# Kernel tuning notes

Measured on AMD Instinct MI355X. Metric: run time of the kernel, lower is better.

## Reference

```python
import jax, jax.numpy as jnp
import numpy as np
from jax import lax

T = 1.0      # terminal time
SIGMA = 1.0  # diffusion coefficient
N, D, P, M, H = 16384, 16, 8, 50, 128


def setup_inputs() -> dict:
    key = jax.random.key(0)
    ks = jax.random.split(key, 8)
    scale1 = 1.0 / np.sqrt(1 + D + P)
    scale2 = 1.0 / np.sqrt(H)
    return {
        "initial_states": jax.random.normal(ks[0], (N, D), jnp.float32),
        "initial_values": jax.random.normal(ks[1], (N,), jnp.float32),
        "observations": jax.random.normal(ks[2], (N, P), jnp.float32),
        "noise": jax.random.normal(ks[3], (M, N, D), jnp.float32),
        "W1": jax.random.normal(ks[4], (1 + D + P, H), jnp.float32) * scale1,
        "b1": jnp.zeros((H,), jnp.float32),
        "W2": jax.random.normal(ks[5], (H, H), jnp.float32) * scale2,
        "b2": jnp.zeros((H,), jnp.float32),
        "W3": jax.random.normal(ks[6], (H, D), jnp.float32) * scale2,
        "b3": jnp.zeros((D,), jnp.float32),
    }


def reference(initial_states, initial_values, observations, noise,
              W1, b1, W2, b2, W3, b3):
    """Euler-Maruyama rollout of simulate_SDEs: joint (X, V) SDE with
    per-step Z-network drift. drift b(X) = -X (OU process)."""
    m_steps = noise.shape[0]
    dt = jnp.asarray(T / m_steps, initial_states.dtype)
    sqrt_dt = jnp.sqrt(dt)
    times = jnp.arange(m_steps, dtype=initial_states.dtype) * dt  # time[m]

    def z_net(t, X, Y):
        tcol = jnp.full((X.shape[0], 1), t, X.dtype)
        h = jnp.concatenate([tcol, X, Y], axis=1)      # (N, 1+d+p)
        h = jax.nn.relu(h @ W1 + b1)
        h = jax.nn.relu(h @ W2 + b2)
        return h @ W3 + b3                             # (N, d)

    def step(carry, inp):
        X, V = carry
        eps, t = inp
        Wn = sqrt_dt * eps                             # Brownian increment
        Z = z_net(t, X, observations)
        drift_V = 0.5 * jnp.sum(Z * Z, axis=1)
        V = V + dt * drift_V + jnp.sum(Z * Wn, axis=1)
        X = X + dt * (-X) + SIGMA * Wn                 # b(X) = -X
        return (X, V), None

    (X, V), _ = lax.scan(step, (initial_states, initial_values), (noise, times))
    return X, V
```

## Files before the change

kernel.cpp:

```cpp
#include <hip/hip_runtime.h>

typedef __bf16   bf16x8 __attribute__((ext_vector_type(8)));
typedef float    f32x4  __attribute__((ext_vector_type(4)));
typedef float    f32x2  __attribute__((ext_vector_type(2)));
typedef uint32_t u32x4  __attribute__((ext_vector_type(4)));

constexpr int N_ = 16384;
constexpr int D_ = 16;
constexpr int P_ = 8;
constexpr int H_ = 128;
constexpr int M_ = 50;

__device__ __forceinline__ uint32_t pk_bf16(float a, float b) {
    uint32_t ua = __builtin_bit_cast(uint32_t, a) + 0x8000u;
    uint32_t ub = __builtin_bit_cast(uint32_t, b) + 0x8000u;
    return __builtin_amdgcn_perm(ub, ua, 0x07060302u);
}
__device__ __forceinline__ uint32_t pk_relu_bf16(float a, float b) {
    return pk_bf16(fmaxf(a, 0.0f), fmaxf(b, 0.0f));
}

__global__ __launch_bounds__(64, 1)
void sde_fused(const float* __restrict__ X0,
               const float* __restrict__ V0,
               const float* __restrict__ Yobs,
               const float* __restrict__ noise,
               const float* __restrict__ W1, const float* __restrict__ b1,
               const float* __restrict__ W2, const float* __restrict__ b2,
               const float* __restrict__ W3, const float* __restrict__ b3,
               float* __restrict__ out)
{
    const int lane = threadIdx.x;
    const int n    = lane & 15;
    const int q    = lane >> 4;
    const int gr   = blockIdx.x * 16 + n;

    const float dt   = 0.02f;
    const float sqdt = 0.1414213562373095f;

    bf16x8 w1f[8];
#pragma unroll
    for (int ct = 0; ct < 8; ++ct) {
        u32x4 u;
        u[0] = pk_bf16(W1[(1 + q * 4 + 0) * H_ + ct * 16 + n],
                       W1[(1 + q * 4 + 1) * H_ + ct * 16 + n]);
        u[1] = pk_bf16(W1[(1 + q * 4 + 2) * H_ + ct * 16 + n],
                       W1[(1 + q * 4 + 3) * H_ + ct * 16 + n]);
        u[2] = pk_bf16(W1[(17 + q * 2 + 0) * H_ + ct * 16 + n],
                       W1[(17 + q * 2 + 1) * H_ + ct * 16 + n]);
        u[3] = (q == 0) ? pk_bf16(b1[ct * 16 + n], W1[ct * 16 + n]) : 0u;
        w1f[ct] = __builtin_bit_cast(bf16x8, u);
    }
    bf16x8 w2f[8][4];
#pragma unroll
    for (int ct = 0; ct < 8; ++ct)
#pragma unroll
        for (int kt = 0; kt < 4; ++kt) {
            u32x4 u;
#pragma unroll
            for (int w = 0; w < 4; ++w) {
                int h0 = (kt * 2 + (w >> 1)) * 16 + q * 4 + (w & 1) * 2;
                u[w] = pk_bf16(W2[h0 * H_ + ct * 16 + n],
                               W2[(h0 + 1) * H_ + ct * 16 + n]);
            }
            w2f[ct][kt] = __builtin_bit_cast(bf16x8, u);
        }
    bf16x8 w3f[4];
#pragma unroll
    for (int kt = 0; kt < 4; ++kt) {
        u32x4 u;
#pragma unroll
        for (int w = 0; w < 4; ++w) {
            int h0 = (kt * 2 + (w >> 1)) * 16 + q * 4 + (w & 1) * 2;
            u[w] = pk_bf16(W3[h0 * D_ + n], W3[(h0 + 1) * D_ + n]);
        }
        w3f[kt] = __builtin_bit_cast(bf16x8, u);
    }
    f32x4 b2r[8];
#pragma unroll
    for (int ct = 0; ct < 8; ++ct)
#pragma unroll
        for (int r = 0; r < 4; ++r) b2r[ct][r] = b2[ct * 16 + q * 4 + r];
    f32x4 b3r;
#pragma unroll
    for (int r = 0; r < 4; ++r) b3r[r] = b3[q * 4 + r];

    f32x4 x = *(const f32x4*)&X0[gr * D_ + q * 4];
    f32x2 y2 = *(const f32x2*)&Yobs[gr * P_ + q * 2];
    const uint32_t yw = pk_bf16(y2[0], y2[1]);

    const float* npb = noise + (size_t)gr * D_ + q * 4;
    f32x4 e0 = *(const f32x4*)npb;
    f32x4 e1 = *(const f32x4*)(npb + (size_t)N_ * D_);
    float t = 0.0f;
    float vacc = 0.0f;

    for (int m = 0; m < M_; ++m) {
        int mp = (m + 2 < M_) ? (m + 2) : (M_ - 1);
        f32x4 e2 = *(const f32x4*)(npb + (size_t)mp * N_ * D_);

        u32x4 au;
        au[0] = pk_bf16(x[0], x[1]);
        au[1] = pk_bf16(x[2], x[3]);
        au[2] = yw;
        au[3] = (q == 0) ? pk_bf16(1.0f, t) : 0u;
        bf16x8 a0 = __builtin_bit_cast(bf16x8, au);

        f32x4 h1c[8];
#pragma unroll
        for (int ct = 0; ct < 8; ++ct)
            h1c[ct] = __builtin_amdgcn_mfma_f32_16x16x32_bf16(
                w1f[ct], a0, (f32x4){0.f, 0.f, 0.f, 0.f}, 0, 0, 0);

        bf16x8 h1b[4];
#pragma unroll
        for (int kt = 0; kt < 4; ++kt) {
            u32x4 u;
            u[0] = pk_relu_bf16(h1c[2 * kt][0], h1c[2 * kt][1]);
            u[1] = pk_relu_bf16(h1c[2 * kt][2], h1c[2 * kt][3]);
            u[2] = pk_relu_bf16(h1c[2 * kt + 1][0], h1c[2 * kt + 1][1]);
            u[3] = pk_relu_bf16(h1c[2 * kt + 1][2], h1c[2 * kt + 1][3]);
            h1b[kt] = __builtin_bit_cast(bf16x8, u);
        }

        f32x4 h2c[8];
#pragma unroll
        for (int ct = 0; ct < 8; ++ct) {
            f32x4 c = b2r[ct];
#pragma unroll
            for (int kt = 0; kt < 4; ++kt)
                c = __builtin_amdgcn_mfma_f32_16x16x32_bf16(w2f[ct][kt], h1b[kt], c, 0, 0, 0);
            h2c[ct] = c;
        }
        bf16x8 h2b[4];
#pragma unroll
        for (int kt = 0; kt < 4; ++kt) {
            u32x4 u;
            u[0] = pk_relu_bf16(h2c[2 * kt][0], h2c[2 * kt][1]);
            u[1] = pk_relu_bf16(h2c[2 * kt][2], h2c[2 * kt][3]);
            u[2] = pk_relu_bf16(h2c[2 * kt + 1][0], h2c[2 * kt + 1][1]);
            u[3] = pk_relu_bf16(h2c[2 * kt + 1][2], h2c[2 * kt + 1][3]);
            h2b[kt] = __builtin_bit_cast(bf16x8, u);
        }

        f32x4 za = __builtin_amdgcn_mfma_f32_16x16x32_bf16(w3f[0], h2b[0], b3r, 0, 0, 0);
        za = __builtin_amdgcn_mfma_f32_16x16x32_bf16(w3f[1], h2b[1], za, 0, 0, 0);
        f32x4 zb = __builtin_amdgcn_mfma_f32_16x16x32_bf16(
            w3f[2], h2b[2], (f32x4){0.f, 0.f, 0.f, 0.f}, 0, 0, 0);
        zb = __builtin_amdgcn_mfma_f32_16x16x32_bf16(w3f[3], h2b[3], zb, 0, 0, 0);

#pragma unroll
        for (int r = 0; r < 4; ++r) {
            float z  = za[r] + zb[r];
            float wn = sqdt * e0[r];
            vacc = fmaf(z, wn, fmaf(0.01f * z, z, vacc));
            x[r] = fmaf(x[r], 0.98f, wn);
        }

        e0 = e1; e1 = e2;
        t += dt;
    }

    float part = vacc;
    part += __shfl_xor(part, 16);
    part += __shfl_xor(part, 32);
    float v = V0[gr] + part;

    *(f32x4*)&out[gr * D_ + q * 4] = x;
    if (q == 0) out[N_ * D_ + gr] = v;
}

extern "C" void kernel_launch(void* const* d_in, const int* in_sizes, int n_in,
                              void* d_out, int out_size, void* d_ws, size_t ws_size,
                              hipStream_t stream)
{
    const float* X0 = (const float*)d_in[0];
    const float* V0 = (const float*)d_in[1];
    const float* Y  = (const float*)d_in[2];
    const float* nz = (const float*)d_in[3];
    const float* W1 = (const float*)d_in[4];
    const float* b1 = (const float*)d_in[5];
    const float* W2 = (const float*)d_in[6];
    const float* b2 = (const float*)d_in[7];
    const float* W3 = (const float*)d_in[8];
    const float* b3 = (const float*)d_in[9];
    float* out = (float*)d_out;

    sde_fused<<<N_ / 16, 64, 0, stream>>>(X0, V0, Y, nz, W1, b1, W2, b2, W3, b3, out);
}
```

Before: 138.1 us.

## Split even/odd timesteps across two waves and stage W2 fragments in LDS

The X recurrence does not depend on the network output, so each block now runs two waves that each redundantly advance X but evaluate the Z-network only on even or odd timesteps. Their V contributions are combined through shared memory at the end. W2 fragments move from registers into a 32 KB LDS table read inside the loop, freeing VGPRs so two blocks can share a CU. This halves the serial MLP chain per wave at the cost of LDS reads on every layer-2 MFMA and duplicated X updates.

```diff
diff --git a/kernel.cpp b/kernel.cpp
--- a/kernel.cpp
+++ b/kernel.cpp
@@ -19,8 +19,16 @@
 __device__ __forceinline__ uint32_t pk_relu_bf16(float a, float b) {
     return pk_bf16(fmaxf(a, 0.0f), fmaxf(b, 0.0f));
 }
-
-__global__ __launch_bounds__(64, 1)
+__device__ __forceinline__ u32x4 pk_frag(f32x4 a, f32x4 b) {
+    u32x4 u;
+    u[0] = pk_relu_bf16(a[0], a[1]);
+    u[1] = pk_relu_bf16(a[2], a[3]);
+    u[2] = pk_relu_bf16(b[0], b[1]);
+    u[3] = pk_relu_bf16(b[2], b[3]);
+    return u;
+}
+
+__global__ __launch_bounds__(128, 2)
 void sde_fused(const float* __restrict__ X0,
                const float* __restrict__ V0,
                const float* __restrict__ Yobs,
@@ -30,13 +38,32 @@
                const float* __restrict__ W3, const float* __restrict__ b3,
                float* __restrict__ out)
 {
-    const int lane = threadIdx.x;
+    __shared__ u32x4 w2lds[32][64];
+    __shared__ float vsh[16];
+
+    const int tid  = threadIdx.x;
+    const int wv   = tid >> 6;
+    const int lane = tid & 63;
     const int n    = lane & 15;
     const int q    = lane >> 4;
     const int gr   = blockIdx.x * 16 + n;
 
     const float dt   = 0.02f;
     const float sqdt = 0.1414213562373095f;
+
+#pragma unroll
+    for (int i = 0; i < 16; ++i) {
+        int idx = wv * 16 + i;
+        int ct = idx >> 2, kt = idx & 3;
+        u32x4 u;
+#pragma unroll
+        for (int w = 0; w < 4; ++w) {
+            int h0 = (kt * 2 + (w >> 1)) * 16 + q * 4 + (w & 1) * 2;
+            u[w] = pk_bf16(W2[h0 * H_ + ct * 16 + n],
+                           W2[(h0 + 1) * H_ + ct * 16 + n]);
+        }
+        w2lds[idx][lane] = u;
+    }
 
     bf16x8 w1f[8];
 #pragma unroll
@@ -51,20 +78,6 @@
         u[3] = (q == 0) ? pk_bf16(b1[ct * 16 + n], W1[ct * 16 + n]) : 0u;
         w1f[ct] = __builtin_bit_cast(bf16x8, u);
     }
-    bf16x8 w2f[8][4];
-#pragma unroll
-    for (int ct = 0; ct < 8; ++ct)
-#pragma unroll
-        for (int kt = 0; kt < 4; ++kt) {
-            u32x4 u;
-#pragma unroll
-            for (int w = 0; w < 4; ++w) {
-                int h0 = (kt * 2 + (w >> 1)) * 16 + q * 4 + (w & 1) * 2;
-                u[w] = pk_bf16(W2[h0 * H_ + ct * 16 + n],
-                               W2[(h0 + 1) * H_ + ct * 16 + n]);
-            }
-            w2f[ct][kt] = __builtin_bit_cast(bf16x8, u);
-        }
     bf16x8 w3f[4];
 #pragma unroll
     for (int kt = 0; kt < 4; ++kt) {
@@ -90,84 +103,96 @@
     const uint32_t yw = pk_bf16(y2[0], y2[1]);
 
     const float* npb = noise + (size_t)gr * D_ + q * 4;
-    f32x4 e0 = *(const f32x4*)npb;
-    f32x4 e1 = *(const f32x4*)(npb + (size_t)N_ * D_);
-    float t = 0.0f;
+    const size_t stp = (size_t)N_ * D_;
+    f32x4 e0 = *(const f32x4*)(npb);
+    f32x4 e1 = *(const f32x4*)(npb + stp);
+    float tw = wv ? dt : 0.0f;
     float vacc = 0.0f;
 
-    for (int m = 0; m < M_; ++m) {
-        int mp = (m + 2 < M_) ? (m + 2) : (M_ - 1);
-        f32x4 e2 = *(const f32x4*)(npb + (size_t)mp * N_ * D_);
+    __syncthreads();
+
+#pragma unroll 1
+    for (int i = 0; i < 25; ++i) {
+        int sa = 2 * i + 2; if (sa > 48) sa = 48;
+        f32x4 pa = *(const f32x4*)(npb + (size_t)sa * stp);
+        f32x4 pb = *(const f32x4*)(npb + (size_t)(sa + 1) * stp);
+
+        f32x4 x1, xin, wnv;
+#pragma unroll
+        for (int r = 0; r < 4; ++r) x1[r] = fmaf(x[r], 0.98f, sqdt * e0[r]);
+#pragma unroll
+        for (int r = 0; r < 4; ++r) {
+            xin[r] = wv ? x1[r] : x[r];
+            wnv[r] = sqdt * (wv ? e1[r] : e0[r]);
+            x[r]   = fmaf(x1[r], 0.98f, sqdt * e1[r]);
+        }
 
         u32x4 au;
-        au[0] = pk_bf16(x[0], x[1]);
-        au[1] = pk_bf16(x[2], x[3]);
+        au[0] = pk_bf16(xin[0], xin[1]);
+        au[1] = pk_bf16(xin[2], xin[3]);
         au[2] = yw;
-        au[3] = (q == 0) ? pk_bf16(1.0f, t) : 0u;
+        au[3] = (q == 0) ? pk_bf16(1.0f, tw) : 0u;
         bf16x8 a0 = __builtin_bit_cast(bf16x8, au);
 
-        f32x4 h1c[8];
-#pragma unroll
-        for (int ct = 0; ct < 8; ++ct)
-            h1c[ct] = __builtin_amdgcn_mfma_f32_16x16x32_bf16(
-                w1f[ct], a0, (f32x4){0.f, 0.f, 0.f, 0.f}, 0, 0, 0);
-
-        bf16x8 h1b[4];
-#pragma unroll
-        for (int kt = 0; kt < 4; ++kt) {
-            u32x4 u;
-            u[0] = pk_relu_bf16(h1c[2 * kt][0], h1c[2 * kt][1]);
-            u[1] = pk_relu_bf16(h1c[2 * kt][2], h1c[2 * kt][3]);
-            u[2] = pk_relu_bf16(h1c[2 * kt + 1][0], h1c[2 * kt + 1][1]);
-            u[3] = pk_relu_bf16(h1c[2 * kt + 1][2], h1c[2 * kt + 1][3]);
-            h1b[kt] = __builtin_bit_cast(bf16x8, u);
-        }
-
-        f32x4 h2c[8];
-#pragma unroll
-        for (int ct = 0; ct < 8; ++ct) {
-            f32x4 c = b2r[ct];
-#pragma unroll
-            for (int kt = 0; kt < 4; ++kt)
-                c = __builtin_amdgcn_mfma_f32_16x16x32_bf16(w2f[ct][kt], h1b[kt], c, 0, 0, 0);
-            h2c[ct] = c;
-        }
-        bf16x8 h2b[4];
-#pragma unroll
-        for (int kt = 0; kt < 4; ++kt) {
-            u32x4 u;
-            u[0] = pk_relu_bf16(h2c[2 * kt][0], h2c[2 * kt][1]);
-            u[1] = pk_relu_bf16(h2c[2 * kt][2], h2c[2 * kt][3]);
-            u[2] = pk_relu_bf16(h2c[2 * kt + 1][0], h2c[2 * kt + 1][1]);
-            u[3] = pk_relu_bf16(h2c[2 * kt + 1][2], h2c[2 * kt + 1][3]);
-            h2b[kt] = __builtin_bit_cast(bf16x8, u);
-        }
-
-        f32x4 za = __builtin_amdgcn_mfma_f32_16x16x32_bf16(w3f[0], h2b[0], b3r, 0, 0, 0);
-        za = __builtin_amdgcn_mfma_f32_16x16x32_bf16(w3f[1], h2b[1], za, 0, 0, 0);
+        f32x4 c0, c1, c2, c3;
+        c0 = __builtin_amdgcn_mfma_f32_16x16x32_bf16(w1f[0], a0, (f32x4){0.f,0.f,0.f,0.f}, 0, 0, 0);
+        c1 = __builtin_amdgcn_mfma_f32_16x16x32_bf16(w1f[1], a0, (f32x4){0.f,0.f,0.f,0.f}, 0, 0, 0);
+        c2 = __builtin_amdgcn_mfma_f32_16x16x32_bf16(w1f[2], a0, (f32x4){0.f,0.f,0.f,0.f}, 0, 0, 0);
+        c3 = __builtin_amdgcn_mfma_f32_16x16x32_bf16(w1f[3], a0, (f32x4){0.f,0.f,0.f,0.f}, 0, 0, 0);
+        bf16x8 h1b0 = __builtin_bit_cast(bf16x8, pk_frag(c0, c1));
+        bf16x8 h1b1 = __builtin_bit_cast(bf16x8, pk_frag(c2, c3));
+        c0 = __builtin_amdgcn_mfma_f32_16x16x32_bf16(w1f[4], a0, (f32x4){0.f,0.f,0.f,0.f}, 0, 0, 0);
+        c1 = __builtin_amdgcn_mfma_f32_16x16x32_bf16(w1f[5], a0, (f32x4){0.f,0.f,0.f,0.f}, 0, 0, 0);
+        c2 = __builtin_amdgcn_mfma_f32_16x16x32_bf16(w1f[6], a0, (f32x4){0.f,0.f,0.f,0.f}, 0, 0, 0);
+        c3 = __builtin_amdgcn_mfma_f32_16x16x32_bf16(w1f[7], a0, (f32x4){0.f,0.f,0.f,0.f}, 0, 0, 0);
+        bf16x8 h1b2 = __builtin_bit_cast(bf16x8, pk_frag(c0, c1));
+        bf16x8 h1b3 = __builtin_bit_cast(bf16x8, pk_frag(c2, c3));
+
+        f32x4 d0, d1, d2, d3;
+#define L2CT(dst, ct)                                                                   \
+        dst = b2r[ct];                                                                  \
+        dst = __builtin_amdgcn_mfma_f32_16x16x32_bf16(                                  \
+            __builtin_bit_cast(bf16x8, w2lds[(ct)*4+0][lane]), h1b0, dst, 0, 0, 0);     \
+        dst = __builtin_amdgcn_mfma_f32_16x16x32_bf16(                                  \
+            __builtin_bit_cast(bf16x8, w2lds[(ct)*4+1][lane]), h1b1, dst, 0, 0, 0);     \
+        dst = __builtin_amdgcn_mfma_f32_16x16x32_bf16(                                  \
+            __builtin_bit_cast(bf16x8, w2lds[(ct)*4+2][lane]), h1b2, dst, 0, 0, 0);     \
+        dst = __builtin_amdgcn_mfma_f32_16x16x32_bf16(                                  \
+            __builtin_bit_cast(bf16x8, w2lds[(ct)*4+3][lane]), h1b3, dst, 0, 0, 0);
+        L2CT(d0, 0) L2CT(d1, 1) L2CT(d2, 2) L2CT(d3, 3)
+        bf16x8 h2b0 = __builtin_bit_cast(bf16x8, pk_frag(d0, d1));
+        bf16x8 h2b1 = __builtin_bit_cast(bf16x8, pk_frag(d2, d3));
+        L2CT(d0, 4) L2CT(d1, 5) L2CT(d2, 6) L2CT(d3, 7)
+        bf16x8 h2b2 = __builtin_bit_cast(bf16x8, pk_frag(d0, d1));
+        bf16x8 h2b3 = __builtin_bit_cast(bf16x8, pk_frag(d2, d3));
+#undef L2CT
+
+        f32x4 za = __builtin_amdgcn_mfma_f32_16x16x32_bf16(w3f[0], h2b0, b3r, 0, 0, 0);
+        za = __builtin_amdgcn_mfma_f32_16x16x32_bf16(w3f[1], h2b1, za, 0, 0, 0);
         f32x4 zb = __builtin_amdgcn_mfma_f32_16x16x32_bf16(
-            w3f[2], h2b[2], (f32x4){0.f, 0.f, 0.f, 0.f}, 0, 0, 0);
-        zb = __builtin_amdgcn_mfma_f32_16x16x32_bf16(w3f[3], h2b[3], zb, 0, 0, 0);
+            w3f[2], h2b2, (f32x4){0.f,0.f,0.f,0.f}, 0, 0, 0);
+        zb = __builtin_amdgcn_mfma_f32_16x16x32_bf16(w3f[3], h2b3, zb, 0, 0, 0);
 
 #pragma unroll
         for (int r = 0; r < 4; ++r) {
-            float z  = za[r] + zb[r];
-            float wn = sqdt * e0[r];
-            vacc = fmaf(z, wn, fmaf(0.01f * z, z, vacc));
-            x[r] = fmaf(x[r], 0.98f, wn);
-        }
-
-        e0 = e1; e1 = e2;
-        t += dt;
+            float z = za[r] + zb[r];
+            vacc = fmaf(z, wnv[r], fmaf(0.01f * z, z, vacc));
+        }
+
+        e0 = pa; e1 = pb;
+        tw += 0.04f;
     }
 
     float part = vacc;
     part += __shfl_xor(part, 16);
     part += __shfl_xor(part, 32);
-    float v = V0[gr] + part;
-
-    *(f32x4*)&out[gr * D_ + q * 4] = x;
-    if (q == 0) out[N_ * D_ + gr] = v;
+    if (wv == 1 && q == 0) vsh[n] = part;
+    __syncthreads();
+
+    if (wv == 0) {
+        *(f32x4*)&out[gr * D_ + q * 4] = x;
+        if (q == 0) out[N_ * D_ + gr] = V0[gr] + part + vsh[n];
+    }
 }
 
 extern "C" void kernel_launch(void* const* d_in, const int* in_sizes, int n_in,
@@ -186,5 +211,5 @@
     const float* b3 = (const float*)d_in[9];
     float* out = (float*)d_out;
 
-    sde_fused<<<N_ / 16, 64, 0, stream>>>(X0, V0, Y, nz, W1, b1, W2, b2, W3, b3, out);
-}
+    sde_fused<<<N_ / 16, 128, 0, stream>>>(X0, V0, Y, nz, W1, b1, W2, b2, W3, b3, out);
+}
```

Result: slower. 161.5 us (+17.0%).
